# Optimization experiments

Hardware: AMD Instinct MI355X
Metric: run time of the kernel (lower is better)

Reference implementation:

```python
import jax, jax.numpy as jnp
import numpy as np

N_NODES = 100000
N_EDGES = 1600000
IN, HID, OUT = 128, 128, 64


def setup_inputs() -> dict:
    key = jax.random.key(0)
    ks = jax.random.split(key, 12)
    x = jax.random.normal(ks[0], (N_NODES, IN), dtype=jnp.float32)
    src = jax.random.randint(ks[1], (N_EDGES,), 0, N_NODES, dtype=jnp.int32)
    dst = jax.random.randint(ks[2], (N_EDGES,), 0, N_NODES, dtype=jnp.int32)

    def lin(k, fan_in, fan_out):
        return jax.random.normal(k, (fan_in, fan_out), dtype=jnp.float32) / jnp.sqrt(jnp.float32(fan_in))

    return {
        "x": x, "src": src, "dst": dst,
        "w_self_0": lin(ks[3], IN, HID), "w_neigh_0": lin(ks[4], IN, HID), "b_0": jnp.zeros((HID,), jnp.float32),
        "w_self_1": lin(ks[5], HID, HID), "w_neigh_1": lin(ks[6], HID, HID), "b_1": jnp.zeros((HID,), jnp.float32),
        "w_self_2": lin(ks[7], HID, OUT), "w_neigh_2": lin(ks[8], HID, OUT), "b_2": jnp.zeros((OUT,), jnp.float32),
    }


def reference(x, src, dst, w_self_0, w_neigh_0, b_0, w_self_1, w_neigh_1, b_1, w_self_2, w_neigh_2, b_2):
    n = x.shape[0]
    # in-degree per dst node; zero-degree nodes keep aggregated 0 (clamp avoids div-by-0)
    deg = jax.ops.segment_sum(jnp.ones_like(dst, dtype=x.dtype), dst, num_segments=n)
    inv_deg = (1.0 / jnp.maximum(deg, 1.0))[:, None]

    def sage_layer(h, w_s, w_n, b):
        # irregular gather of src features, segment-mean over dst
        agg = jax.ops.segment_sum(h[src], dst, num_segments=n) * inv_deg
        return h @ w_s + agg @ w_n + b

    h = jax.nn.relu(sage_layer(x, w_self_0, w_neigh_0, b_0))   # dropout = identity (eval)
    h = jax.nn.relu(sage_layer(h, w_self_1, w_neigh_1, b_1))
    return sage_layer(h, w_self_2, w_neigh_2, b_2)
```

## Files before the change

### kernel.cpp

```cpp
#include <hip/hip_runtime.h>


#define NN 100000
#define NE 1600000
#define BSH 7
#define BND 128
#define NB  782
#define NBLKS 256
#define EPB ((NE + NBLKS - 1) / NBLKS)
#define STOT (NB * NBLKS)
#define SCAN_E 2048
#define NSB ((STOT + SCAN_E - 1) / SCAN_E)
#define GEMM0_BLOCKS 782
#define KMAX 6

typedef __attribute__((ext_vector_type(8))) short short8;
typedef __attribute__((ext_vector_type(4))) float f32x4;
typedef unsigned int uint;
typedef unsigned short ushort;

__device__ inline ushort f2bf(float f) {
    uint u = __float_as_uint(f);
    u += 0x7FFFu + ((u >> 16) & 1u);
    return (ushort)(u >> 16);
}
__device__ inline float bf_lo(uint w) { return __uint_as_float(w << 16); }
__device__ inline float bf_hi(uint w) { return __uint_as_float(w & 0xFFFF0000u); }

template<int NCS, int NCN, bool XF32, bool ABF>
__device__ void gemm_body(int wid, int tid,
    const void* __restrict__ Hv, const short8* __restrict__ wp,
    const float* __restrict__ bias, void* __restrict__ Av, ushort* __restrict__ Bt)
{
    constexpr int NCT = (NCS + NCN) / 16;
    if (wid >= NN / 16) return;
    const int lane = tid & 63;
    const int m = lane & 15;
    const int q = lane >> 4;

    short8 af[4];
    if (XF32) {
        const float* hp = (const float*)Hv + (size_t)(wid * 16 + m) * 128;
        #pragma unroll
        for (int kt = 0; kt < 4; ++kt) {
            const float4 f0 = *(const float4*)(hp + kt * 32 + q * 8);
            const float4 f1 = *(const float4*)(hp + kt * 32 + q * 8 + 4);
            short8 v;
            v[0] = (short)f2bf(f0.x); v[1] = (short)f2bf(f0.y);
            v[2] = (short)f2bf(f0.z); v[3] = (short)f2bf(f0.w);
            v[4] = (short)f2bf(f1.x); v[5] = (short)f2bf(f1.y);
            v[6] = (short)f2bf(f1.z); v[7] = (short)f2bf(f1.w);
            af[kt] = v;
        }
    } else {
        const short8* hp = (const short8*)((const ushort*)Hv + (size_t)(wid * 16 + m) * 128);
        #pragma unroll
        for (int kt = 0; kt < 4; ++kt) af[kt] = hp[kt * 4 + q];
    }

    f32x4 acc[NCT];
    #pragma unroll
    for (int i = 0; i < NCT; ++i) acc[i] = (f32x4){0.f, 0.f, 0.f, 0.f};

    #pragma unroll
    for (int ct = 0; ct < NCT; ++ct) {
        #pragma unroll
        for (int kt = 0; kt < 4; ++kt) {
            const short8 bf = wp[(ct * 4 + kt) * 64 + lane];
            acc[ct] = __builtin_amdgcn_mfma_f32_16x16x32_bf16(af[kt], bf, acc[ct], 0, 0, 0);
        }
    }

    const int r0 = wid * 16 + q * 4;
    #pragma unroll
    for (int ct = 0; ct < NCS / 16; ++ct) {
        const int c = ct * 16 + m;
        const float bv = bias[c];
        #pragma unroll
        for (int r = 0; r < 4; ++r) {
            const float v = acc[ct][r] + bv;
            if (ABF) ((ushort*)Av)[(size_t)(r0 + r) * NCS + c] = f2bf(v);
            else     ((float*) Av)[(size_t)(r0 + r) * NCS + c] = v;
        }
    }
    #pragma unroll
    for (int ct = NCS / 16; ct < NCT; ++ct) {
        const int c = ct * 16 + m - NCS;
        #pragma unroll
        for (int r = 0; r < 4; ++r)
            Bt[(size_t)(r0 + r) * NCN + c] = f2bf(acc[ct][r]);
    }
}

template<int NCS, int NCN, bool XF32, bool ABF>
__global__ __launch_bounds__(512) void gemm_mfma_k(
    const void* __restrict__ Hv, const ushort* __restrict__ Wf,
    const float* __restrict__ bias, void* __restrict__ Av, ushort* __restrict__ Bt)
{
    constexpr int NCT = (NCS + NCN) / 16;
    __shared__ short8 wl[NCT * 4 * 64];
    uint4* dl = (uint4*)wl;
    const uint4* sg = (const uint4*)Wf;
    for (int i = threadIdx.x; i < NCT * 4 * 64; i += 512) dl[i] = sg[i];
    __syncthreads();
    gemm_body<NCS, NCN, XF32, ABF>(
        (blockIdx.x * 512 + threadIdx.x) >> 6, threadIdx.x, Hv, wl, bias, Av, Bt);
}

__global__ __launch_bounds__(256) void phist_pack_k(
    const int* __restrict__ dst, int* __restrict__ histG,
    const float* __restrict__ ws0, const float* __restrict__ wn0, ushort* __restrict__ wf0,
    const float* __restrict__ ws1, const float* __restrict__ wn1, ushort* __restrict__ wf1,
    const float* __restrict__ ws2, const float* __restrict__ wn2, ushort* __restrict__ wf2)
{
    __shared__ int h[NB];
    const int t = threadIdx.x;
    if (blockIdx.x < NBLKS) {
        for (int i = t; i < NB; i += 256) h[i] = 0;
        __syncthreads();
        const int blk = blockIdx.x;
        const int e0 = blk * EPB;
        const int2* dp = (const int2*)(dst + e0);
        for (int k = t; k < EPB / 2; k += 256) {
            const int2 d2 = dp[k];
            atomicAdd(&h[d2.x >> BSH], 1);
            atomicAdd(&h[d2.y >> BSH], 1);
        }
        __syncthreads();
        for (int i = t; i < NB; i += 256)
            histG[i * NBLKS + blk] = h[i];
        return;
    }
    const int b = blockIdx.x - NBLKS;
    const float *ws, *wn; ushort* wf; int ncs, idx;
    if (b < 16)      { ws = ws0; wn = wn0; wf = wf0; ncs = 128; idx = b * 256 + t; }
    else if (b < 32) { ws = ws1; wn = wn1; wf = wf1; ncs = 128; idx = (b - 16) * 256 + t; }
    else             { ws = ws2; wn = wn2; wf = wf2; ncs = 64;  idx = (b - 32) * 256 + t; }
    const int total = (2 * ncs / 16) * 4 * 64;
    if (idx >= total) return;
    const int l = idx & 63;
    const int f = idx >> 6;
    const int kt = f & 3;
    const int ct = f >> 2;
    const int n = ct * 16 + (l & 15);
    const int k0 = kt * 32 + (l >> 4) * 8;
    uint w[4];
    #pragma unroll
    for (int p = 0; p < 4; ++p) {
        const int k = k0 + p * 2;
        float v0, v1;
        if (n < ncs) { v0 = ws[k * ncs + n];         v1 = ws[(k + 1) * ncs + n]; }
        else         { v0 = wn[k * ncs + (n - ncs)]; v1 = wn[(k + 1) * ncs + (n - ncs)]; }
        w[p] = (uint)f2bf(v0) | ((uint)f2bf(v1) << 16);
    }
    uint4 o; o.x = w[0]; o.y = w[1]; o.z = w[2]; o.w = w[3];
    ((uint4*)wf)[idx] = o;
}

__global__ __launch_bounds__(256) void scan1_k(int* __restrict__ data, int* __restrict__ blksum) {
    __shared__ int lds[256];
    const int t = threadIdx.x;
    const int base = blockIdx.x * SCAN_E + t * 8;
    int v[8];
    int s = 0;
    #pragma unroll
    for (int i = 0; i < 8; ++i) {
        const int idx = base + i;
        v[i] = (idx < STOT) ? data[idx] : 0;
        s += v[i];
    }
    lds[t] = s;
    __syncthreads();
    #pragma unroll
    for (int off = 1; off < 256; off <<= 1) {
        const int cur = lds[t];
        const int y = (t >= off) ? lds[t - off] : 0;
        __syncthreads();
        lds[t] = cur + y;
        __syncthreads();
    }
    const int incl = lds[t];
    if (t == 255) blksum[blockIdx.x] = incl;
    int run = incl - s;
    #pragma unroll
    for (int i = 0; i < 8; ++i) {
        const int idx = base + i;
        if (idx < STOT) data[idx] = run;
        run += v[i];
    }
}

__global__ __launch_bounds__(256) void scan3_k(int* __restrict__ data, const int* __restrict__ blksum) {
    __shared__ int lds[256];
    const int t = threadIdx.x;
    lds[t] = (t < NSB) ? blksum[t] : 0;
    __syncthreads();
    #pragma unroll
    for (int off = 1; off < 256; off <<= 1) {
        const int cur = lds[t];
        const int y = (t >= off) ? lds[t - off] : 0;
        __syncthreads();
        lds[t] = cur + y;
        __syncthreads();
    }
    const int add = (blockIdx.x == 0) ? 0 : lds[blockIdx.x - 1];
    const int base = blockIdx.x * SCAN_E + t * 8;
    #pragma unroll
    for (int i = 0; i < 8; ++i) {
        const int idx = base + i;
        if (idx < STOT) data[idx] += add;
    }
}

__global__ __launch_bounds__(512) void pscatter_k(
    const int* __restrict__ src, const int* __restrict__ dst,
    const int* __restrict__ histG, int* __restrict__ pb)
{
    __shared__ int wc[NB];
    const int t = threadIdx.x;
    const int blk = blockIdx.x;
    for (int i = t; i < NB; i += 512) wc[i] = histG[i * NBLKS + blk];
    __syncthreads();
    const int e0 = blk * EPB;
    const int2* dp = (const int2*)(dst + e0);
    const int2* sp = (const int2*)(src + e0);
    for (int k = t; k < EPB / 2; k += 512) {
        const int2 d2 = dp[k];
        const int2 s2 = sp[k];
        const int p0 = atomicAdd(&wc[d2.x >> BSH], 1);
        pb[p0] = (s2.x << BSH) | (d2.x & (BND - 1));
        const int p1 = atomicAdd(&wc[d2.y >> BSH], 1);
        pb[p1] = (s2.y << BSH) | (d2.y & (BND - 1));
    }
}

__global__ __launch_bounds__(512) void bucketgemm0_k(
    const int* __restrict__ histG, const int* __restrict__ pb,
    int* __restrict__ row, int* __restrict__ esrc,
    const float* __restrict__ x, const ushort* __restrict__ wf0,
    const float* __restrict__ b0, ushort* __restrict__ Abf, ushort* __restrict__ Bt)
{
    __shared__ uint4 sh[4096];
    const int t = threadIdx.x;
    if (blockIdx.x < NB) {
        int* cnt  = (int*)sh;
        int* wc   = cnt + BND;
        int* excl = wc + BND;
        int* scn  = excl + BND;
        const int b = blockIdx.x;
        if (t < BND) { cnt[t] = 0; wc[t] = 0; }
        __syncthreads();
        const int s0 = histG[b * NBLKS];
        const int s1 = (b + 1 < NB) ? histG[(b + 1) * NBLKS] : NE;
        const int n = s1 - s0;
        int held[KMAX];
        const bool fits = (n <= KMAX * 512);
        if (fits) {
            #pragma unroll
            for (int i = 0; i < KMAX; ++i) {
                const int e = s0 + t + i * 512;
                held[i] = (e < s1) ? pb[e] : -1;
            }
            #pragma unroll
            for (int i = 0; i < KMAX; ++i)
                if (held[i] >= 0) atomicAdd(&cnt[held[i] & (BND - 1)], 1);
        } else {
            for (int e = s0 + t; e < s1; e += 512)
                atomicAdd(&cnt[pb[e] & (BND - 1)], 1);
        }
        __syncthreads();
        if (t < BND) scn[t] = cnt[t];
        __syncthreads();
        for (int off = 1; off < BND; off <<= 1) {
            int nv = 0;
            if (t < BND) {
                nv = scn[t];
                if (t >= off) nv += scn[t - off];
            }
            __syncthreads();
            if (t < BND) scn[t] = nv;
            __syncthreads();
        }
        if (t < BND) {
            const int ex = scn[t] - cnt[t];
            excl[t] = ex;
            const int node = b * BND + t;
            if (node <= NN) row[node] = s0 + ex;
        }
        __syncthreads();
        if (fits) {
            #pragma unroll
            for (int i = 0; i < KMAX; ++i) {
                if (held[i] >= 0) {
                    const int p = held[i];
                    const int dl = p & (BND - 1);
                    const int pos = s0 + excl[dl] + atomicAdd(&wc[dl], 1);
                    esrc[pos] = p >> BSH;
                }
            }
        } else {
            for (int e = s0 + t; e < s1; e += 512) {
                const int p = pb[e];
                const int dl = p & (BND - 1);
                const int pos = s0 + excl[dl] + atomicAdd(&wc[dl], 1);
                esrc[pos] = p >> BSH;
            }
        }
        return;
    }
    const uint4* sg = (const uint4*)wf0;
    for (int i = t; i < 4096; i += 512) sh[i] = sg[i];
    __syncthreads();
    gemm_body<128, 128, true, true>(
        ((blockIdx.x - NB) * 512 + t) >> 6, t, x, (const short8*)sh, b0, Abf, Bt);
}

__global__ __launch_bounds__(256) void agg128_k(
    const int* __restrict__ row, const int* __restrict__ esrc,
    const ushort* __restrict__ Bt, const ushort* __restrict__ Abf, ushort* __restrict__ Hb)
{
    const int w = (blockIdx.x * 256 + threadIdx.x) >> 6;
    const int half = (threadIdx.x >> 5) & 1;
    const int ln = threadIdx.x & 31;
    const int node = w * 2 + half;
    if (node >= NN) return;
    const int e0 = row[node];
    const int e1 = row[node + 1];
    const uint2* B = (const uint2*)Bt;
    float a0 = 0.f, a1 = 0.f, a2 = 0.f, a3 = 0.f;
    int e = e0;
    for (; e + 8 <= e1; e += 8) {
        int s[8];
        #pragma unroll
        for (int j = 0; j < 8; ++j) s[j] = esrc[e + j];
        uint2 v[8];
        #pragma unroll
        for (int j = 0; j < 8; ++j) v[j] = B[(size_t)s[j] * 32 + ln];
        #pragma unroll
        for (int j = 0; j < 8; ++j) {
            a0 += bf_lo(v[j].x); a1 += bf_hi(v[j].x);
            a2 += bf_lo(v[j].y); a3 += bf_hi(v[j].y);
        }
    }
    for (; e + 2 <= e1; e += 2) {
        const int s0 = esrc[e], s1 = esrc[e + 1];
        const uint2 v0 = B[(size_t)s0 * 32 + ln];
        const uint2 v1 = B[(size_t)s1 * 32 + ln];
        a0 += bf_lo(v0.x) + bf_lo(v1.x); a1 += bf_hi(v0.x) + bf_hi(v1.x);
        a2 += bf_lo(v0.y) + bf_lo(v1.y); a3 += bf_hi(v0.y) + bf_hi(v1.y);
    }
    if (e < e1) {
        const uint2 v = B[(size_t)esrc[e] * 32 + ln];
        a0 += bf_lo(v.x); a1 += bf_hi(v.x);
        a2 += bf_lo(v.y); a3 += bf_hi(v.y);
    }
    const int deg = e1 - e0;
    const float invd = (deg > 0) ? 1.0f / (float)deg : 0.0f;
    const uint2 aw = ((const uint2*)Abf)[(size_t)node * 32 + ln];
    const float v0 = fmaxf(bf_lo(aw.x) + a0 * invd, 0.f);
    const float v1 = fmaxf(bf_hi(aw.x) + a1 * invd, 0.f);
    const float v2 = fmaxf(bf_lo(aw.y) + a2 * invd, 0.f);
    const float v3 = fmaxf(bf_hi(aw.y) + a3 * invd, 0.f);
    uint2 o;
    o.x = (uint)f2bf(v0) | ((uint)f2bf(v1) << 16);
    o.y = (uint)f2bf(v2) | ((uint)f2bf(v3) << 16);
    ((uint2*)Hb)[(size_t)node * 32 + ln] = o;
}

__global__ __launch_bounds__(256) void agg64_k(
    const int* __restrict__ row, const int* __restrict__ esrc,
    const ushort* __restrict__ Bt, float* __restrict__ out)
{
    const int node = (blockIdx.x * 256 + threadIdx.x) >> 4;
    const int ln = threadIdx.x & 15;
    if (node >= NN) return;
    const int e0 = row[node];
    const int e1 = row[node + 1];
    const uint2* B = (const uint2*)Bt;
    float a0 = 0.f, a1 = 0.f, a2 = 0.f, a3 = 0.f;
    int e = e0;
    for (; e + 8 <= e1; e += 8) {
        int s[8];
        #pragma unroll
        for (int j = 0; j < 8; ++j) s[j] = esrc[e + j];
        uint2 v[8];
        #pragma unroll
        for (int j = 0; j < 8; ++j) v[j] = B[(size_t)s[j] * 16 + ln];
        #pragma unroll
        for (int j = 0; j < 8; ++j) {
            a0 += bf_lo(v[j].x); a1 += bf_hi(v[j].x);
            a2 += bf_lo(v[j].y); a3 += bf_hi(v[j].y);
        }
    }
    for (; e + 2 <= e1; e += 2) {
        const int s0 = esrc[e], s1 = esrc[e + 1];
        const uint2 v0 = B[(size_t)s0 * 16 + ln];
        const uint2 v1 = B[(size_t)s1 * 16 + ln];
        a0 += bf_lo(v0.x) + bf_lo(v1.x); a1 += bf_hi(v0.x) + bf_hi(v1.x);
        a2 += bf_lo(v0.y) + bf_lo(v1.y); a3 += bf_hi(v0.y) + bf_hi(v1.y);
    }
    if (e < e1) {
        const uint2 v = B[(size_t)esrc[e] * 16 + ln];
        a0 += bf_lo(v.x); a1 += bf_hi(v.x);
        a2 += bf_lo(v.y); a3 += bf_hi(v.y);
    }
    const int deg = e1 - e0;
    const float invd = (deg > 0) ? 1.0f / (float)deg : 0.0f;
    float4* op = (float4*)(out + (size_t)node * 64 + ln * 4);
    float4 o = *op;
    o.x += a0 * invd; o.y += a1 * invd;
    o.z += a2 * invd; o.w += a3 * invd;
    *op = o;
}

__device__ inline float4 relu4f(float4 v) {
    v.x = fmaxf(v.x, 0.f); v.y = fmaxf(v.y, 0.f);
    v.z = fmaxf(v.z, 0.f); v.w = fmaxf(v.w, 0.f);
    return v;
}
template<int NCOL, bool RELU_IN, bool BIAS>
__global__ __launch_bounds__(256) void gemm_k(
    const float* in, const float* __restrict__ W,
    const float* __restrict__ bias, float* out)
{
    constexpr int K = 128;
    constexpr int QUADS = NCOL / 4;
    constexpr int G = 256 / QUADS;
    constexpr int RPT = 32 / G;
    __shared__ float Wlds[K * NCOL];
    {
        const float4* Wg = reinterpret_cast<const float4*>(W);
        float4* Wl = reinterpret_cast<float4*>(Wlds);
        #pragma unroll
        for (int i = 0; i < K * NCOL / 4 / 256; ++i)
            Wl[threadIdx.x + i * 256] = Wg[threadIdx.x + i * 256];
    }
    __syncthreads();
    const int tx = threadIdx.x % QUADS;
    const int ty = threadIdx.x / QUADS;
    const int row0 = blockIdx.x * 32;
    const float* rp[RPT];
    #pragma unroll
    for (int i = 0; i < RPT; ++i) rp[i] = in + (size_t)(row0 + ty + i * G) * K;
    float acc[RPT][4];
    #pragma unroll
    for (int i = 0; i < RPT; ++i) acc[i][0] = acc[i][1] = acc[i][2] = acc[i][3] = 0.f;
    #pragma unroll 2
    for (int kc = 0; kc < K; kc += 4) {
        float4 h4[RPT];
        #pragma unroll
        for (int i = 0; i < RPT; ++i) {
            h4[i] = *reinterpret_cast<const float4*>(rp[i] + kc);
            if (RELU_IN) h4[i] = relu4f(h4[i]);
        }
        #pragma unroll
        for (int kk = 0; kk < 4; ++kk) {
            const float4 w4 = *reinterpret_cast<const float4*>(&Wlds[(kc + kk) * NCOL + tx * 4]);
            #pragma unroll
            for (int i = 0; i < RPT; ++i) {
                const float hv = (&h4[i].x)[kk];
                acc[i][0] = fmaf(hv, w4.x, acc[i][0]);
                acc[i][1] = fmaf(hv, w4.y, acc[i][1]);
                acc[i][2] = fmaf(hv, w4.z, acc[i][2]);
                acc[i][3] = fmaf(hv, w4.w, acc[i][3]);
            }
        }
    }
    float4 b4 = make_float4(0.f, 0.f, 0.f, 0.f);
    if (BIAS) b4 = *reinterpret_cast<const float4*>(&bias[tx * 4]);
    #pragma unroll
    for (int i = 0; i < RPT; ++i) {
        const int r = row0 + ty + i * G;
        float4 o;
        o.x = acc[i][0] + b4.x; o.y = acc[i][1] + b4.y;
        o.z = acc[i][2] + b4.z; o.w = acc[i][3] + b4.w;
        *reinterpret_cast<float4*>(&out[(size_t)r * NCOL + tx * 4]) = o;
    }
}
__global__ void deg_k(const int* __restrict__ dst, float* __restrict__ deg, int E) {
    const int i = blockIdx.x * blockDim.x + threadIdx.x;
    if (i < E) atomicAdd(&deg[dst[i]], 1.0f);
}
__global__ void inv_k(float* deg, int n) {
    const int i = blockIdx.x * blockDim.x + threadIdx.x;
    if (i < n) deg[i] = 1.0f / fmaxf(deg[i], 1.0f);
}
__global__ __launch_bounds__(256) void scatter128_k(
    const int* __restrict__ src, const int* __restrict__ dst,
    const float* __restrict__ inv, const float* __restrict__ B, float* A, int E) {
    const int lane = threadIdx.x & 63;
    int w = (blockIdx.x * 256 + threadIdx.x) >> 6;
    const int nw = (gridDim.x * 256) >> 6;
    for (int e = w; e < E; e += nw) {
        const int s = src[e], d = dst[e];
        const float sc = inv[d];
        const float2 v = *reinterpret_cast<const float2*>(&B[(size_t)s * 128 + lane * 2]);
        atomicAdd(&A[(size_t)d * 128 + lane * 2    ], v.x * sc);
        atomicAdd(&A[(size_t)d * 128 + lane * 2 + 1], v.y * sc);
    }
}
__global__ __launch_bounds__(256) void scatter64_k(
    const int* __restrict__ src, const int* __restrict__ dst,
    const float* __restrict__ inv, const float* __restrict__ B, float* A, int E) {
    const int lane = threadIdx.x & 63;
    int w = (blockIdx.x * 256 + threadIdx.x) >> 6;
    const int nw = (gridDim.x * 256) >> 6;
    for (int e = w; e < E; e += nw) {
        const int s = src[e], d = dst[e];
        atomicAdd(&A[(size_t)d * 64 + lane], B[(size_t)s * 64 + lane] * inv[d]);
    }
}

extern "C" void kernel_launch(void* const* d_in, const int* in_sizes, int n_in,
                              void* d_out, int out_size, void* d_ws, size_t ws_size,
                              hipStream_t stream) {
    const float* x   = (const float*)d_in[0];
    const int*   src = (const int*)  d_in[1];
    const int*   dst = (const int*)  d_in[2];
    const float* ws0 = (const float*)d_in[3];
    const float* wn0 = (const float*)d_in[4];
    const float* b0  = (const float*)d_in[5];
    const float* ws1 = (const float*)d_in[6];
    const float* wn1 = (const float*)d_in[7];
    const float* b1  = (const float*)d_in[8];
    const float* ws2 = (const float*)d_in[9];
    const float* wn2 = (const float*)d_in[10];
    const float* b2  = (const float*)d_in[11];
    float* out = (float*)d_out;

    const size_t O_BLK  = 4096;
    const size_t O_ROW  = 16384;
    const size_t O_WF0  = 417792;
    const size_t O_WF1  = 483328;
    const size_t O_WF2  = 548864;
    const size_t O_ESRC = 581632;
    const size_t O_PB   = 6983680;
    const size_t O_A    = 14286848;
    const size_t O_BT   = 39890944;
    const size_t O_HB   = 65495040;
    const size_t NEED   = 91095040;

    if (ws_size >= NEED) {
        int*    blks  = (int*)   ((char*)d_ws + O_BLK);
        int*    row   = (int*)   ((char*)d_ws + O_ROW);
        ushort* wf0   = (ushort*)((char*)d_ws + O_WF0);
        ushort* wf1   = (ushort*)((char*)d_ws + O_WF1);
        ushort* wf2   = (ushort*)((char*)d_ws + O_WF2);
        int*    esrc  = (int*)   ((char*)d_ws + O_ESRC);
        int*    pb    = (int*)   ((char*)d_ws + O_PB);
        ushort* Abf   = (ushort*)((char*)d_ws + O_A);
        ushort* Bt    = (ushort*)((char*)d_ws + O_BT);
        ushort* Hb    = (ushort*)((char*)d_ws + O_HB);
        int*    histG = (int*)   ((char*)d_ws + O_HB);

        phist_pack_k<<<NBLKS + 40, 256, 0, stream>>>(dst, histG,
            ws0, wn0, wf0, ws1, wn1, wf1, ws2, wn2, wf2);
        scan1_k<<<NSB, 256, 0, stream>>>(histG, blks);
        scan3_k<<<NSB, 256, 0, stream>>>(histG, blks);
        pscatter_k<<<NBLKS, 512, 0, stream>>>(src, dst, histG, pb);
        bucketgemm0_k<<<NB + GEMM0_BLOCKS, 512, 0, stream>>>(
            histG, pb, row, esrc, x, wf0, b0, Abf, Bt);

        const int AGG128_BLOCKS = (NN / 2 + 3) / 4;
        const int A64B = (NN + 15) / 16;
        const int GEMM512_BLOCKS = (NN / 16 + 7) / 8;

        agg128_k<<<AGG128_BLOCKS, 256, 0, stream>>>(row, esrc, Bt, Abf, Hb);
        gemm_mfma_k<128, 128, false, true ><<<GEMM512_BLOCKS, 512, 0, stream>>>(Hb, wf1, b1, Abf, Bt);
        agg128_k<<<AGG128_BLOCKS, 256, 0, stream>>>(row, esrc, Bt, Abf, Hb);
        gemm_mfma_k<64, 64, false, false><<<GEMM512_BLOCKS, 512, 0, stream>>>(Hb, wf2, b2, out, Bt);
        agg64_k<<<A64B, 256, 0, stream>>>(row, esrc, Bt, out);
    } else {
        float* inv = (float*)d_ws;
        float* H0  = (float*)((char*)d_ws + (1u << 20));
        float* Bf  = H0 + (size_t)NN * 128;
        const int GB = NN / 32;
        const int SC_BLOCKS = 4096;
        hipMemsetAsync(inv, 0, NN * sizeof(float), stream);
        deg_k<<<(NE + 255) / 256, 256, 0, stream>>>(dst, inv, NE);
        inv_k<<<(NN + 255) / 256, 256, 0, stream>>>(inv, NN);
        gemm_k<128, false, false><<<GB, 256, 0, stream>>>(x, wn0, nullptr, Bf);
        gemm_k<128, false, true ><<<GB, 256, 0, stream>>>(x, ws0, b0, H0);
        scatter128_k<<<SC_BLOCKS, 256, 0, stream>>>(src, dst, inv, Bf, H0, NE);
        gemm_k<128, true, false><<<GB, 256, 0, stream>>>(H0, wn1, nullptr, Bf);
        gemm_k<128, true, true ><<<GB, 256, 0, stream>>>(H0, ws1, b1, H0);
        scatter128_k<<<SC_BLOCKS, 256, 0, stream>>>(src, dst, inv, Bf, H0, NE);
        gemm_k<64, true, false><<<GB, 256, 0, stream>>>(H0, wn2, nullptr, Bf);
        gemm_k<64, true, true ><<<GB, 256, 0, stream>>>(H0, ws2, b2, out);
        scatter64_k<<<SC_BLOCKS, 256, 0, stream>>>(src, dst, inv, Bf, out, NE);
    }
}
```

Measured before the change: 353.2 us.

## Spread layer-0 GEMM blocks across histogram, scatter and bucket kernels

The layer-0 dense GEMM used to run only inside the bucket-sort kernel. It is now split into three chunks (150, 240 and the remaining blocks) that run as extra blocks in the histogram, partial-scatter and bucket kernels. The aim is to fill the GPU while those atomic-heavy, low-occupancy sort phases run. Weight packing moves to its own small kernel ahead of them so the GEMM blocks have packed weights ready. This adds one launch, and the histogram now uses 512-thread blocks with a large shared buffer, which may lower occupancy for the sort blocks.

```diff
diff --git a/kernel.cpp b/kernel.cpp
--- a/kernel.cpp
+++ b/kernel.cpp
@@ -12,6 +12,9 @@
 #define SCAN_E 2048
 #define NSB ((STOT + SCAN_E - 1) / SCAN_E)
 #define GEMM0_BLOCKS 782
+#define GA 150
+#define GB 240
+#define GC (GEMM0_BLOCKS - GA - GB)
 #define KMAX 6
 
 typedef __attribute__((ext_vector_type(8))) short short8;
@@ -107,31 +110,24 @@
         (blockIdx.x * 512 + threadIdx.x) >> 6, threadIdx.x, Hv, wl, bias, Av, Bt);
 }
 
-__global__ __launch_bounds__(256) void phist_pack_k(
-    const int* __restrict__ dst, int* __restrict__ histG,
+__device__ inline void gemm0_role(uint4* sh, int chunk_blk, int t,
+    const float* __restrict__ x, const ushort* __restrict__ wf0,
+    const float* __restrict__ b0, ushort* __restrict__ Abf, ushort* __restrict__ Bt)
+{
+    const uint4* sg = (const uint4*)wf0;
+    for (int i = t; i < 4096; i += 512) sh[i] = sg[i];
+    __syncthreads();
+    gemm_body<128, 128, true, true>(chunk_blk * 8 + (t >> 6), t, x,
+                                    (const short8*)sh, b0, Abf, Bt);
+}
+
+__global__ __launch_bounds__(256) void pack_k(
     const float* __restrict__ ws0, const float* __restrict__ wn0, ushort* __restrict__ wf0,
     const float* __restrict__ ws1, const float* __restrict__ wn1, ushort* __restrict__ wf1,
     const float* __restrict__ ws2, const float* __restrict__ wn2, ushort* __restrict__ wf2)
 {
-    __shared__ int h[NB];
     const int t = threadIdx.x;
-    if (blockIdx.x < NBLKS) {
-        for (int i = t; i < NB; i += 256) h[i] = 0;
-        __syncthreads();
-        const int blk = blockIdx.x;
-        const int e0 = blk * EPB;
-        const int2* dp = (const int2*)(dst + e0);
-        for (int k = t; k < EPB / 2; k += 256) {
-            const int2 d2 = dp[k];
-            atomicAdd(&h[d2.x >> BSH], 1);
-            atomicAdd(&h[d2.y >> BSH], 1);
-        }
-        __syncthreads();
-        for (int i = t; i < NB; i += 256)
-            histG[i * NBLKS + blk] = h[i];
-        return;
-    }
-    const int b = blockIdx.x - NBLKS;
+    const int b = blockIdx.x;
     const float *ws, *wn; ushort* wf; int ncs, idx;
     if (b < 16)      { ws = ws0; wn = wn0; wf = wf0; ncs = 128; idx = b * 256 + t; }
     else if (b < 32) { ws = ws1; wn = wn1; wf = wf1; ncs = 128; idx = (b - 16) * 256 + t; }
@@ -157,6 +153,33 @@
     ((uint4*)wf)[idx] = o;
 }
 
+__global__ __launch_bounds__(512) void phist_gemm0_k(
+    const int* __restrict__ dst, int* __restrict__ histG,
+    const float* __restrict__ x, const ushort* __restrict__ wf0,
+    const float* __restrict__ b0, ushort* __restrict__ Abf, ushort* __restrict__ Bt)
+{
+    __shared__ uint4 sh[4096];
+    const int t = threadIdx.x;
+    if (blockIdx.x < NBLKS) {
+        int* h = (int*)sh;
+        for (int i = t; i < NB; i += 512) h[i] = 0;
+        __syncthreads();
+        const int blk = blockIdx.x;
+        const int e0 = blk * EPB;
+        const int2* dp = (const int2*)(dst + e0);
+        for (int k = t; k < EPB / 2; k += 512) {
+            const int2 d2 = dp[k];
+            atomicAdd(&h[d2.x >> BSH], 1);
+            atomicAdd(&h[d2.y >> BSH], 1);
+        }
+        __syncthreads();
+        for (int i = t; i < NB; i += 512)
+            histG[i * NBLKS + blk] = h[i];
+        return;
+    }
+    gemm0_role(sh, blockIdx.x - NBLKS, t, x, wf0, b0, Abf, Bt);
+}
+
 __global__ __launch_bounds__(256) void scan1_k(int* __restrict__ data, int* __restrict__ blksum) {
     __shared__ int lds[256];
     const int t = threadIdx.x;
@@ -212,29 +235,36 @@
     }
 }
 
-__global__ __launch_bounds__(512) void pscatter_k(
+__global__ __launch_bounds__(512) void pscatter_gemm0_k(
     const int* __restrict__ src, const int* __restrict__ dst,
-    const int* __restrict__ histG, int* __restrict__ pb)
-{
-    __shared__ int wc[NB];
+    const int* __restrict__ histG, int* __restrict__ pb,
+    const float* __restrict__ x, const ushort* __restrict__ wf0,
+    const float* __restrict__ b0, ushort* __restrict__ Abf, ushort* __restrict__ Bt)
+{
+    __shared__ uint4 sh[4096];
     const int t = threadIdx.x;
-    const int blk = blockIdx.x;
-    for (int i = t; i < NB; i += 512) wc[i] = histG[i * NBLKS + blk];
-    __syncthreads();
-    const int e0 = blk * EPB;
-    const int2* dp = (const int2*)(dst + e0);
-    const int2* sp = (const int2*)(src + e0);
-    for (int k = t; k < EPB / 2; k += 512) {
-        const int2 d2 = dp[k];
-        const int2 s2 = sp[k];
-        const int p0 = atomicAdd(&wc[d2.x >> BSH], 1);
-        pb[p0] = (s2.x << BSH) | (d2.x & (BND - 1));
-        const int p1 = atomicAdd(&wc[d2.y >> BSH], 1);
-        pb[p1] = (s2.y << BSH) | (d2.y & (BND - 1));
-    }
-}
-
-__global__ __launch_bounds__(512) void bucketgemm0_k(
+    if (blockIdx.x < NBLKS) {
+        int* wc = (int*)sh;
+        const int blk = blockIdx.x;
+        for (int i = t; i < NB; i += 512) wc[i] = histG[i * NBLKS + blk];
+        __syncthreads();
+        const int e0 = blk * EPB;
+        const int2* dp = (const int2*)(dst + e0);
+        const int2* sp = (const int2*)(src + e0);
+        for (int k = t; k < EPB / 2; k += 512) {
+            const int2 d2 = dp[k];
+            const int2 s2 = sp[k];
+            const int p0 = atomicAdd(&wc[d2.x >> BSH], 1);
+            pb[p0] = (s2.x << BSH) | (d2.x & (BND - 1));
+            const int p1 = atomicAdd(&wc[d2.y >> BSH], 1);
+            pb[p1] = (s2.y << BSH) | (d2.y & (BND - 1));
+        }
+        return;
+    }
+    gemm0_role(sh, GA + blockIdx.x - NBLKS, t, x, wf0, b0, Abf, Bt);
+}
+
+__global__ __launch_bounds__(512) void bucket_gemm0_k(
     const int* __restrict__ histG, const int* __restrict__ pb,
     int* __restrict__ row, int* __restrict__ esrc,
     const float* __restrict__ x, const ushort* __restrict__ wf0,
@@ -308,11 +338,7 @@
         }
         return;
     }
-    const uint4* sg = (const uint4*)wf0;
-    for (int i = t; i < 4096; i += 512) sh[i] = sg[i];
-    __syncthreads();
-    gemm_body<128, 128, true, true>(
-        ((blockIdx.x - NB) * 512 + t) >> 6, t, x, (const short8*)sh, b0, Abf, Bt);
+    gemm0_role(sh, GA + GB + blockIdx.x - NB, t, x, wf0, b0, Abf, Bt);
 }
 
 __global__ __launch_bounds__(256) void agg128_k(
@@ -553,12 +579,13 @@
         ushort* Hb    = (ushort*)((char*)d_ws + O_HB);
         int*    histG = (int*)   ((char*)d_ws + O_HB);
 
-        phist_pack_k<<<NBLKS + 40, 256, 0, stream>>>(dst, histG,
-            ws0, wn0, wf0, ws1, wn1, wf1, ws2, wn2, wf2);
+        pack_k<<<40, 256, 0, stream>>>(ws0, wn0, wf0, ws1, wn1, wf1, ws2, wn2, wf2);
+        phist_gemm0_k<<<NBLKS + GA, 512, 0, stream>>>(dst, histG, x, wf0, b0, Abf, Bt);
         scan1_k<<<NSB, 256, 0, stream>>>(histG, blks);
         scan3_k<<<NSB, 256, 0, stream>>>(histG, blks);
-        pscatter_k<<<NBLKS, 512, 0, stream>>>(src, dst, histG, pb);
-        bucketgemm0_k<<<NB + GEMM0_BLOCKS, 512, 0, stream>>>(
+        pscatter_gemm0_k<<<NBLKS + GB, 512, 0, stream>>>(
+            src, dst, histG, pb, x, wf0, b0, Abf, Bt);
+        bucket_gemm0_k<<<NB + GC, 512, 0, stream>>>(
             histG, pb, row, esrc, x, wf0, b0, Abf, Bt);
 
         const int AGG128_BLOCKS = (NN / 2 + 3) / 4;
@@ -574,19 +601,19 @@
         float* inv = (float*)d_ws;
         float* H0  = (float*)((char*)d_ws + (1u << 20));
         float* Bf  = H0 + (size_t)NN * 128;
-        const int GB = NN / 32;
+        const int GB2 = NN / 32;
         const int SC_BLOCKS = 4096;
         hipMemsetAsync(inv, 0, NN * sizeof(float), stream);
         deg_k<<<(NE + 255) / 256, 256, 0, stream>>>(dst, inv, NE);
         inv_k<<<(NN + 255) / 256, 256, 0, stream>>>(inv, NN);
-        gemm_k<128, false, false><<<GB, 256, 0, stream>>>(x, wn0, nullptr, Bf);
-        gemm_k<128, false, true ><<<GB, 256, 0, stream>>>(x, ws0, b0, H0);
+        gemm_k<128, false, false><<<GB2, 256, 0, stream>>>(x, wn0, nullptr, Bf);
+        gemm_k<128, false, true ><<<GB2, 256, 0, stream>>>(x, ws0, b0, H0);
         scatter128_k<<<SC_BLOCKS, 256, 0, stream>>>(src, dst, inv, Bf, H0, NE);
-        gemm_k<128, true, false><<<GB, 256, 0, stream>>>(H0, wn1, nullptr, Bf);
-        gemm_k<128, true, true ><<<GB, 256, 0, stream>>>(H0, ws1, b1, H0);
+        gemm_k<128, true, false><<<GB2, 256, 0, stream>>>(H0, wn1, nullptr, Bf);
+        gemm_k<128, true, true ><<<GB2, 256, 0, stream>>>(H0, ws1, b1, H0);
         scatter128_k<<<SC_BLOCKS, 256, 0, stream>>>(src, dst, inv, Bf, H0, NE);
-        gemm_k<64, true, false><<<GB, 256, 0, stream>>>(H0, wn2, nullptr, Bf);
-        gemm_k<64, true, true ><<<GB, 256, 0, stream>>>(H0, ws2, b2, out);
+        gemm_k<64, true, false><<<GB2, 256, 0, stream>>>(H0, wn2, nullptr, Bf);
+        gemm_k<64, true, true ><<<GB2, 256, 0, stream>>>(H0, ws2, b2, out);
         scatter64_k<<<SC_BLOCKS, 256, 0, stream>>>(src, dst, inv, Bf, out, NE);
     }
 }
```

New measurement: 384.1 us. 8.7% more time.
